# Performance work log

Measured on AMD Instinct MI355X. Metric: run time of the kernel, lower is better.

The kernel has to match this reference:

```python
import jax, jax.numpy as jnp
import numpy as np


def setup_inputs() -> dict:
    A, F, C = 9, 128, 20          # anchors per cell, feature map size, num classes
    B, L = 32, 64                 # batch, num GT labels
    N = A * F * F                 # total anchors
    rng = np.random.default_rng(0)
    # label_data rows: (class, cx, cy, w, h); boxes strictly positive for log()
    lcls = rng.integers(0, C, L)
    lbox = rng.uniform(8.0, 100.0, (L, 4))
    label_data = np.concatenate([lcls[:, None].astype(np.float64), lbox], axis=1).astype(np.float32)
    # occurrence index of each label within its class (matches the inner count loop)
    occ = np.array([int(np.sum(lcls[:l] == lcls[l])) for l in range(L)])
    # anchor_data rows: (id, class, cx, cy, w, h, occurrence)
    a = np.zeros((N, 7), np.float32)
    a[:, 0] = np.arange(N)
    a[:, 1] = C  # background by default
    a[:, 2:6] = rng.uniform(8.0, 100.0, (N, 4))
    pos_idx = rng.choice(N, 128, replace=False)
    lab_pick = rng.integers(0, L, 128)
    a[pos_idx, 1] = lcls[lab_pick]
    a[pos_idx, 6] = occ[lab_pick]
    ign = rng.choice(np.setdiff1d(np.arange(N), pos_idx), 256, replace=False)
    a[ign, 1] = -1.0  # ignored anchors
    # deterministic stand-in for random.sample(range(N), 300) per batch element
    neg_samples = np.stack([rng.choice(N, 300, replace=False) for _ in range(B)]).astype(np.int32)
    k1, k2 = jax.random.split(jax.random.key(0))
    return {
        "cla_map": jax.random.normal(k1, (B, 2 * A, F, F), jnp.float32),
        "reg_map": jax.random.normal(k2, (B, 4 * A, F, F), jnp.float32),
        "label_data": jnp.asarray(label_data),
        "anchor_data": jnp.asarray(a),
        "neg_samples": jnp.asarray(neg_samples),
        "num_anchors": A,
        "fmap_size": F,
        "num_classes": C,
    }


def _smooth_l1(d):
    ad = jnp.abs(d)
    return jnp.where(ad < 1.0, 0.5 * d * d, ad - 0.5)


def reference(cla_map, reg_map, label_data, anchor_data, neg_samples, num_anchors, fmap_size, num_classes):
    A, F, C = num_anchors, fmap_size, num_classes
    B = cla_map.shape[0]
    N = anchor_data.shape[0]
    L = label_data.shape[0]

    a_lbl = anchor_data[:, 1]
    a_box = anchor_data[:, 2:6]          # cx, cy, w, h
    a_occ = anchor_data[:, 6]
    pos_mask = (a_lbl != -1.0) & (a_lbl != C)   # [N]

    # per-label occurrence index within its class (replaces inner label loop)
    l_cls = label_data[:, 0]
    li = jnp.arange(L)
    occ = jnp.sum((l_cls[None, :] == l_cls[:, None]) & (li[None, :] < li[:, None]), axis=1)  # [L]
    match = (l_cls[None, :] == a_lbl[:, None]) & (occ[None, :].astype(a_occ.dtype) == a_occ[:, None])  # [N,L]
    gt_idx = jnp.argmax(match, axis=1)
    g = label_data[gt_idx]               # [N,5]

    t = jnp.stack([
        (g[:, 1] - a_box[:, 0]) / a_box[:, 2],
        (g[:, 2] - a_box[:, 1]) / a_box[:, 3],
        jnp.log(g[:, 3] / a_box[:, 2]),
        jnp.log(g[:, 4] / a_box[:, 3]),
    ], axis=1)                           # [N,4]

    # anchor -> (channel, h, w) mapping, exactly as in the torch loops
    i = jnp.arange(N)
    h = (i // A) % F
    w = (i // A) // F
    c4 = (i % A) * 4
    c2 = (i % A) * 2

    p_reg = reg_map[:, c4[:, None] + jnp.arange(4)[None, :], h[:, None], w[:, None]]  # [B,N,4]
    p_cls = cla_map[:, c2[:, None] + jnp.arange(2)[None, :], h[:, None], w[:, None]]  # [B,N,2]

    loss_reg = jnp.mean(_smooth_l1(p_reg - t[None]), axis=-1)            # [B,N] SmoothL1 mean over 4
    loss_cls_pos = -jax.nn.log_softmax(p_cls, axis=-1)[..., 1]           # CE with soft target [0,1]
    pos_loss = jnp.sum(jnp.where(pos_mask[None, :], loss_cls_pos + 4.0 * loss_reg, 0.0))
    P = jnp.sum(pos_mask)                # positive count (same for every batch element)

    # negatives: walk sampled indices, take background anchors until count >= 3*P
    is_neg = a_lbl[neg_samples] == C                     # [B,300]
    cum = jnp.cumsum(is_neg.astype(jnp.int32), axis=1)
    include = is_neg & (cum <= 3 * P)                    # [B,300]
    nh, nw, nc2 = h[neg_samples], w[neg_samples], c2[neg_samples]
    npc = cla_map[jnp.arange(B)[:, None, None],
                  nc2[:, :, None] + jnp.arange(2)[None, None, :],
                  nh[:, :, None], nw[:, :, None]]        # [B,300,2]
    neg_loss = -jax.nn.log_softmax(npc, axis=-1)[..., 0] # CE with soft target [1,0]
    neg_total = jnp.sum(jnp.where(include, neg_loss, 0.0))
    neg_count = jnp.sum(include)

    denom = (B * P + neg_count).astype(cla_map.dtype)
    return ((pos_loss + neg_total) / denom).reshape(1)
```

## Files before the change

kernel.cpp:

```cpp
#include <hip/hip_runtime.h>
#include <math.h>

#define MAXL 256

struct __align__(16) PosRec {
    float t0, t1, t2, t3;
    int c2, h, w, pad;
};

__global__ void __launch_bounds__(256)
k_scan(const float* __restrict__ anchor,
       const float* __restrict__ label,
       const int* __restrict__ dA,
       const int* __restrict__ dF,
       const int* __restrict__ dC,
       int N, int L, int maxRec,
       int* __restrict__ cnt,
       PosRec* __restrict__ recs)
{
    const int A = *dA;
    const int F = *dF;
    const float Cf = (float)(*dC);

    __shared__ float sh_cls[MAXL];
    __shared__ int   sh_occ[MAXL];
    const bool useLds = (L <= MAXL);
    if (useLds) {
        for (int j = threadIdx.x; j < L; j += blockDim.x)
            sh_cls[j] = label[(size_t)j * 5];
        __syncthreads();
        for (int j = threadIdx.x; j < L; j += blockDim.x) {
            float c = sh_cls[j];
            int o = 0;
            for (int k = 0; k < j; ++k) o += (sh_cls[k] == c) ? 1 : 0;
            sh_occ[j] = o;
        }
        __syncthreads();
    }

    const int tid = blockIdx.x * blockDim.x + threadIdx.x;
    const int nth = gridDim.x * blockDim.x;

    for (int n = tid; n < N; n += nth) {
        float albl = anchor[(size_t)n * 7 + 1];
        if (albl == -1.0f || albl == Cf) continue;

        float ax   = anchor[(size_t)n * 7 + 2];
        float ay   = anchor[(size_t)n * 7 + 3];
        float aw   = anchor[(size_t)n * 7 + 4];
        float ah   = anchor[(size_t)n * 7 + 5];
        float aocc = anchor[(size_t)n * 7 + 6];

        int gt = 0;
        for (int j = 0; j < L; ++j) {
            float cj; int oj;
            if (useLds) { cj = sh_cls[j]; oj = sh_occ[j]; }
            else {
                cj = label[(size_t)j * 5];
                oj = 0;
                for (int k = 0; k < j; ++k) oj += (label[(size_t)k * 5] == cj) ? 1 : 0;
            }
            if (cj == albl && (float)oj == aocc) { gt = j; break; }
        }
        const float* g = label + (size_t)gt * 5;

        PosRec r;
        r.t0 = (g[1] - ax) / aw;
        r.t1 = (g[2] - ay) / ah;
        r.t2 = logf(g[3] / aw);
        r.t3 = logf(g[4] / ah);
        int tmp = n / A;
        int ai  = n - tmp * A;
        r.h = tmp % F;
        r.w = tmp / F;
        r.c2 = ai * 2;
        r.pad = 0;

        int slot = atomicAdd(cnt, 1);
        if (slot < maxRec) recs[slot] = r;
    }
}

#define POS_BLOCKS 16
#define NEG_BLOCKS 8

__global__ void __launch_bounds__(256)
k_loss(const float* __restrict__ cla,
       const float* __restrict__ reg,
       const float* __restrict__ anchor,
       const int* __restrict__ neg,
       const int* __restrict__ dA,
       const int* __restrict__ dF,
       const int* __restrict__ dC,
       int B, int S,
       const int* __restrict__ cnt,
       const PosRec* __restrict__ recs,
       double* __restrict__ pos_loss,
       double* __restrict__ neg_loss,
       int* __restrict__ neg_cnt)
{
    const int A = *dA;
    const int F = *dF;
    const size_t hw = (size_t)F * F;
    const int P = *cnt;
    const int lane = threadIdx.x & 63;

    if (blockIdx.x < POS_BLOCKS) {
        const int tid = blockIdx.x * blockDim.x + threadIdx.x;
        const int nth = POS_BLOCKS * blockDim.x;
        const int T = P * B;

        double acc = 0.0;
        for (int task = tid; task < T; task += nth) {
            int p = task / B;
            int b = task - p * B;
            PosRec r = recs[p];
            int c4 = r.c2 * 2;

            size_t regBase = (((size_t)b * (4 * A) + c4) * F + r.h) * F + r.w;
            float d0 = reg[regBase]          - r.t0;
            float d1 = reg[regBase +     hw] - r.t1;
            float d2 = reg[regBase + 2 * hw] - r.t2;
            float d3 = reg[regBase + 3 * hw] - r.t3;

            float lr = 0.0f, ad;
            ad = fabsf(d0); lr += (ad < 1.0f) ? 0.5f * d0 * d0 : ad - 0.5f;
            ad = fabsf(d1); lr += (ad < 1.0f) ? 0.5f * d1 * d1 : ad - 0.5f;
            ad = fabsf(d2); lr += (ad < 1.0f) ? 0.5f * d2 * d2 : ad - 0.5f;
            ad = fabsf(d3); lr += (ad < 1.0f) ? 0.5f * d3 * d3 : ad - 0.5f;
            lr *= 0.25f;

            size_t claBase = (((size_t)b * (2 * A) + r.c2) * F + r.h) * F + r.w;
            float x0 = cla[claBase];
            float x1 = cla[claBase + hw];
            float m  = fmaxf(x0, x1);
            float lse = m + logf(expf(x0 - m) + expf(x1 - m));

            acc += (double)((lse - x1) + 4.0f * lr);
        }
        for (int off = 32; off > 0; off >>= 1) acc += __shfl_down(acc, off, 64);
        if (lane == 0 && acc != 0.0) atomicAdd(pos_loss, acc);
    } else {
        const float Cf = (float)(*dC);
        int gwave = (blockIdx.x - POS_BLOCKS) * (blockDim.x >> 6) + (threadIdx.x >> 6);
        if (gwave >= B) return;
        int b = gwave;
        const int limit = 3 * P;

        int base = 0;
        float lsum = 0.0f;
        int lcnt = 0;
        for (int c0 = 0; c0 < S; c0 += 64) {
            int s = c0 + lane;
            bool valid = (s < S);
            int idx   = valid ? neg[(size_t)b * S + s] : 0;
            float lbl = valid ? anchor[(size_t)idx * 7 + 1] : -2.0f;
            bool isneg = valid && (lbl == Cf);

            unsigned long long mask = __ballot(isneg);
            int pre = __popcll(mask & ((1ull << lane) - 1ull));
            int cum = base + pre + (isneg ? 1 : 0);

            if (isneg && cum <= limit) {
                int tmp = idx / A;
                int ai  = idx - tmp * A;
                int h   = tmp % F;
                int w2  = tmp / F;
                size_t claBase = (((size_t)b * (2 * A) + ai * 2) * F + h) * F + w2;
                float x0 = cla[claBase];
                float x1 = cla[claBase + hw];
                float m  = fmaxf(x0, x1);
                lsum += m + logf(expf(x0 - m) + expf(x1 - m)) - x0;
                lcnt += 1;
            }
            base += __popcll(mask);
        }
        for (int off = 32; off > 0; off >>= 1) {
            lsum += __shfl_down(lsum, off, 64);
            lcnt += __shfl_down(lcnt, off, 64);
        }
        if (lane == 0 && lcnt != 0) {
            atomicAdd(neg_loss, (double)lsum);
            atomicAdd(neg_cnt, lcnt);
        }
    }
}

__global__ void k_final(const int* __restrict__ cnt,
                        const int* __restrict__ neg_cnt,
                        const double* __restrict__ pos_loss,
                        const double* __restrict__ neg_loss,
                        int B,
                        float* __restrict__ out)
{
    double denom = (double)(B * (*cnt) + (*neg_cnt));
    out[0] = (float)((*pos_loss + *neg_loss) / denom);
}

extern "C" void kernel_launch(void* const* d_in, const int* in_sizes, int n_in,
                              void* d_out, int out_size, void* d_ws, size_t ws_size,
                              hipStream_t stream) {
    const float* cla    = (const float*)d_in[0];
    const float* reg    = (const float*)d_in[1];
    const float* label  = (const float*)d_in[2];
    const float* anchor = (const float*)d_in[3];
    const int*   neg    = (const int*)d_in[4];
    const int*   dA     = (const int*)d_in[5];
    const int*   dF     = (const int*)d_in[6];
    const int*   dC     = (const int*)d_in[7];

    int N = in_sizes[3] / 7;
    int L = in_sizes[2] / 5;
    int B = in_sizes[0] / (2 * N);
    int S = in_sizes[4] / B;

    char* ws = (char*)d_ws;
    int*    cnt      = (int*)(ws + 0);
    int*    neg_cnt  = (int*)(ws + 4);
    double* pos_loss = (double*)(ws + 16);
    double* neg_loss = (double*)(ws + 24);
    PosRec* recs     = (PosRec*)(ws + 64);
    int maxRec = (int)((ws_size - 64) / sizeof(PosRec));

    hipMemsetAsync(ws, 0, 64, stream);

    int scanGrid = 128;
    k_scan<<<scanGrid, 256, 0, stream>>>(anchor, label, dA, dF, dC,
                                         N, L, maxRec, cnt, recs);

    int negBlocks = (B + 3) / 4;
    int lossGrid = POS_BLOCKS + (negBlocks > NEG_BLOCKS ? negBlocks : NEG_BLOCKS);
    k_loss<<<lossGrid, 256, 0, stream>>>(cla, reg, anchor, neg, dA, dF, dC,
                                         B, S, cnt, recs,
                                         pos_loss, neg_loss, neg_cnt);

    k_final<<<1, 1, 0, stream>>>(cnt, neg_cnt, pos_loss, neg_loss, B,
                                 (float*)d_out);
}
```

Baseline: 157.1 us.

## Fuse final reduction into loss kernel and batch negative-sample loads

Removes the separate single-thread finalize kernel by having the last block to finish (tracked with an atomic done counter) compute the output, which saves one launch. The negative-sample path now loads up to 8 chunks of indices and labels into registers before doing the ballot scan, so the dependent gathers overlap. The cla loads become unconditional for valid samples. The scan grid is doubled and the positive count is clamped to maxRec. The cost is some extra wasted cla loads and a threadfence and atomic per block.

```diff
diff --git a/kernel.cpp b/kernel.cpp
--- a/kernel.cpp
+++ b/kernel.cpp
@@ -82,7 +82,7 @@
 }
 
 #define POS_BLOCKS 16
-#define NEG_BLOCKS 8
+#define CMAX 8
 
 __global__ void __launch_bounds__(256)
 k_loss(const float* __restrict__ cla,
@@ -92,12 +92,14 @@
        const int* __restrict__ dA,
        const int* __restrict__ dF,
        const int* __restrict__ dC,
-       int B, int S,
-       const int* __restrict__ cnt,
+       int B, int S, int maxRec,
+       int* __restrict__ cnt,
        const PosRec* __restrict__ recs,
        double* __restrict__ pos_loss,
        double* __restrict__ neg_loss,
-       int* __restrict__ neg_cnt)
+       int* __restrict__ neg_cnt,
+       int* __restrict__ done,
+       float* __restrict__ out)
 {
     const int A = *dA;
     const int F = *dF;
@@ -108,7 +110,8 @@
     if (blockIdx.x < POS_BLOCKS) {
         const int tid = blockIdx.x * blockDim.x + threadIdx.x;
         const int nth = POS_BLOCKS * blockDim.x;
-        const int T = P * B;
+        int Pc = (P < maxRec) ? P : maxRec;
+        const int T = Pc * B;
 
         double acc = 0.0;
         for (int task = tid; task < T; task += nth) {
@@ -143,58 +146,75 @@
     } else {
         const float Cf = (float)(*dC);
         int gwave = (blockIdx.x - POS_BLOCKS) * (blockDim.x >> 6) + (threadIdx.x >> 6);
-        if (gwave >= B) return;
-        int b = gwave;
-        const int limit = 3 * P;
-
-        int base = 0;
-        float lsum = 0.0f;
-        int lcnt = 0;
-        for (int c0 = 0; c0 < S; c0 += 64) {
-            int s = c0 + lane;
-            bool valid = (s < S);
-            int idx   = valid ? neg[(size_t)b * S + s] : 0;
-            float lbl = valid ? anchor[(size_t)idx * 7 + 1] : -2.0f;
-            bool isneg = valid && (lbl == Cf);
-
-            unsigned long long mask = __ballot(isneg);
-            int pre = __popcll(mask & ((1ull << lane) - 1ull));
-            int cum = base + pre + (isneg ? 1 : 0);
-
-            if (isneg && cum <= limit) {
-                int tmp = idx / A;
-                int ai  = idx - tmp * A;
-                int h   = tmp % F;
-                int w2  = tmp / F;
-                size_t claBase = (((size_t)b * (2 * A) + ai * 2) * F + h) * F + w2;
-                float x0 = cla[claBase];
-                float x1 = cla[claBase + hw];
-                float m  = fmaxf(x0, x1);
-                lsum += m + logf(expf(x0 - m) + expf(x1 - m)) - x0;
-                lcnt += 1;
-            }
-            base += __popcll(mask);
-        }
-        for (int off = 32; off > 0; off >>= 1) {
-            lsum += __shfl_down(lsum, off, 64);
-            lcnt += __shfl_down(lcnt, off, 64);
-        }
-        if (lane == 0 && lcnt != 0) {
-            atomicAdd(neg_loss, (double)lsum);
-            atomicAdd(neg_cnt, lcnt);
-        }
-    }
-}
-
-__global__ void k_final(const int* __restrict__ cnt,
-                        const int* __restrict__ neg_cnt,
-                        const double* __restrict__ pos_loss,
-                        const double* __restrict__ neg_loss,
-                        int B,
-                        float* __restrict__ out)
-{
-    double denom = (double)(B * (*cnt) + (*neg_cnt));
-    out[0] = (float)((*pos_loss + *neg_loss) / denom);
+        if (gwave < B) {
+            int b = gwave;
+            const int limit = 3 * P;
+            const unsigned long long lanemask = (1ull << lane) - 1ull;
+
+            int base = 0;
+            float lsum = 0.0f;
+            int lcnt = 0;
+
+            for (int g0 = 0; g0 < S; g0 += 64 * CMAX) {
+                int   idxr[CMAX];
+                float lblr[CMAX];
+
+                #pragma unroll
+                for (int c = 0; c < CMAX; ++c) {
+                    int s = g0 + c * 64 + lane;
+                    idxr[c] = (s < S) ? neg[(size_t)b * S + s] : 0;
+                }
+                #pragma unroll
+                for (int c = 0; c < CMAX; ++c) {
+                    int s = g0 + c * 64 + lane;
+                    lblr[c] = (s < S) ? anchor[(size_t)idxr[c] * 7 + 1] : -2.0f;
+                }
+                #pragma unroll
+                for (int c = 0; c < CMAX; ++c) {
+                    int s = g0 + c * 64 + lane;
+                    bool valid = (s < S);
+                    bool isneg = valid && (lblr[c] == Cf);
+                    unsigned long long mask = __ballot(isneg);
+                    int pre = __popcll(mask & lanemask);
+                    int cum = base + pre + (isneg ? 1 : 0);
+                    bool inc = isneg && (cum <= limit);
+                    base += __popcll(mask);
+
+                    int idx = idxr[c];
+                    int tmp = idx / A;
+                    int ai  = idx - tmp * A;
+                    int h   = tmp % F;
+                    int w2  = tmp / F;
+                    size_t claBase = (((size_t)b * (2 * A) + ai * 2) * F + h) * F + w2;
+                    float x0 = valid ? cla[claBase]      : 0.0f;
+                    float x1 = valid ? cla[claBase + hw] : 0.0f;
+                    float m  = fmaxf(x0, x1);
+                    float l  = m + logf(expf(x0 - m) + expf(x1 - m)) - x0;
+                    lsum += inc ? l : 0.0f;
+                    lcnt += inc ? 1 : 0;
+                }
+            }
+            for (int off = 32; off > 0; off >>= 1) {
+                lsum += __shfl_down(lsum, off, 64);
+                lcnt += __shfl_down(lcnt, off, 64);
+            }
+            if (lane == 0 && lcnt != 0) {
+                atomicAdd(neg_loss, (double)lsum);
+                atomicAdd(neg_cnt, lcnt);
+            }
+        }
+    }
+
+    __syncthreads();
+    if (threadIdx.x == 0) {
+        __threadfence();
+        int t = atomicAdd(done, 1);
+        if (t == (int)gridDim.x - 1) {
+            __threadfence();
+            double denom = (double)(B * P + *neg_cnt);
+            out[0] = (float)((*pos_loss + *neg_loss) / denom);
+        }
+    }
 }
 
 extern "C" void kernel_launch(void* const* d_in, const int* in_sizes, int n_in,
@@ -217,6 +237,7 @@
     char* ws = (char*)d_ws;
     int*    cnt      = (int*)(ws + 0);
     int*    neg_cnt  = (int*)(ws + 4);
+    int*    done     = (int*)(ws + 8);
     double* pos_loss = (double*)(ws + 16);
     double* neg_loss = (double*)(ws + 24);
     PosRec* recs     = (PosRec*)(ws + 64);
@@ -224,16 +245,14 @@
 
     hipMemsetAsync(ws, 0, 64, stream);
 
-    int scanGrid = 128;
+    int scanGrid = 256;
     k_scan<<<scanGrid, 256, 0, stream>>>(anchor, label, dA, dF, dC,
                                          N, L, maxRec, cnt, recs);
 
     int negBlocks = (B + 3) / 4;
-    int lossGrid = POS_BLOCKS + (negBlocks > NEG_BLOCKS ? negBlocks : NEG_BLOCKS);
+    int lossGrid = POS_BLOCKS + negBlocks;
     k_loss<<<lossGrid, 256, 0, stream>>>(cla, reg, anchor, neg, dA, dF, dC,
-                                         B, S, cnt, recs,
-                                         pos_loss, neg_loss, neg_cnt);
-
-    k_final<<<1, 1, 0, stream>>>(cnt, neg_cnt, pos_loss, neg_loss, B,
-                                 (float*)d_out);
+                                         B, S, maxRec, cnt, recs,
+                                         pos_loss, neg_loss, neg_cnt, done,
+                                         (float*)d_out);
 }
```

Result: faster. 153.5 us (-2.3%).
